# Performance work log

Hardware: AMD Instinct MI355X
Metric: run time of the kernel (lower is better)

## Reference

```python
import jax, jax.numpy as jnp
import numpy as np
from jax import lax

N_CLASS = 20
N_BOX = 2
GRID = 56          # n_cell_hw derived from input width: 56*56*(2*5+20) = 94080
BATCH = 256
SCORE_THRESH = 0.1 # hard-coded in _preds_filte
IOU_THRESH = 0.4   # hard-coded in _preds_filte
MAX_OUT = 30       # max_output_size
NMS_CAND = 256     # pre-select top candidates per image before O(K^2) NMS


def setup_inputs() -> dict:
    key = jax.random.key(0)
    D = GRID * GRID * (N_BOX * 5 + N_CLASS)
    net_outs = jax.random.uniform(key, (BATCH, D), dtype=jnp.float32)
    return {"net_outs": net_outs}


def _decode(net_outs):
    # Faithful port of _net_outs_parse (wh_sqrt=True)
    B = net_outs.shape[0]
    S, nb, C = GRID, N_BOX, N_CLASS
    bd1 = C * S * S
    bd2 = bd1 + nb * S * S
    cell_c = net_outs[:, :bd1].reshape(B, S, S, C)
    conf = net_outs[:, bd1:bd2].reshape(B, S, S, nb)
    coord = net_outs[:, bd2:].reshape(B, S, S, nb, 4)
    t_xy, t_wh = coord[..., :2], coord[..., 2:]
    # mesh_grid: w_index varies along axis 1, h_index along axis 0, stacked as (w, h)
    X, Y = jnp.meshgrid(jnp.arange(S, dtype=net_outs.dtype),
                        jnp.arange(S, dtype=net_outs.dtype), indexing='xy')
    grid = jnp.stack([X, Y], axis=-1)[:, :, None, :]  # [S,S,1,2]
    xy = (t_xy + grid) / S
    wh = jnp.square(t_wh)  # wh_sqrt=True
    mn = xy - wh * 0.5
    mx = xy + wh * 0.5
    # boxes_corner = [ymin, xmin, ymax, xmax]
    corners = jnp.concatenate([mn[..., 1:2], mn[..., 0:1], mx[..., 1:2], mx[..., 0:1]], axis=-1)
    c_probs = jnp.broadcast_to(cell_c[:, :, :, None, :], (B, S, S, nb, C))
    return jnp.concatenate([corners, conf[..., None], c_probs], axis=-1)  # [B,S,S,nb,5+C]


def _pairwise_iou(b):
    ymin, xmin, ymax, xmax = b[:, 0], b[:, 1], b[:, 2], b[:, 3]
    area = jnp.maximum(ymax - ymin, 0.0) * jnp.maximum(xmax - xmin, 0.0)
    iy = jnp.maximum(0.0, jnp.minimum(ymax[:, None], ymax[None, :]) - jnp.maximum(ymin[:, None], ymin[None, :]))
    ix = jnp.maximum(0.0, jnp.minimum(xmax[:, None], xmax[None, :]) - jnp.maximum(xmin[:, None], xmin[None, :]))
    inter = iy * ix
    union = area[:, None] + area[None, :] - inter
    return jnp.where(union > 0.0, inter / union, 0.0)


def _nms_image(item):
    # item: [N, 6] = (ymin, xmin, ymax, xmax, score, class)
    scores = item[:, 4]
    _, top_i = lax.top_k(scores, NMS_CAND)   # candidate pre-selection (greedy NMS only ever picks highest scores)
    cand = item[top_i]                       # [K, 6]
    iou = _pairwise_iou(cand[:, :4])         # [K, K]
    neg = jnp.finfo(item.dtype).min

    def step(valid, _):
        m = jnp.where(valid, cand[:, 4], neg)
        idx = jnp.argmax(m)
        ok = valid[idx]
        valid = valid & (iou[idx] <= IOU_THRESH)
        valid = valid.at[idx].set(False)
        return valid, (idx, ok)

    _, (idxs, ok) = lax.scan(step, jnp.ones(NMS_CAND, dtype=bool), None, length=MAX_OUT)
    rows = cand[idxs] * ok[:, None].astype(item.dtype)  # invalid slots -> zero rows (== pad with 0)
    _, oi = lax.top_k(rows[:, 4], MAX_OUT)               # sort by score desc, like tf.nn.top_k on padded preds
    return rows[oi]


def reference(net_outs):
    preds = _decode(net_outs)                    # [B,S,S,nb,25]
    B = preds.shape[0]
    cls_score = preds[..., 4:5] * preds[..., 5:]  # conf * class probs  [B,S,S,nb,C]
    cls = jnp.argmax(cls_score, axis=-1).astype(preds.dtype)
    s = jnp.max(cls_score, axis=-1)
    s = jnp.where(s >= SCORE_THRESH, s, 0.0)
    items = jnp.concatenate([preds[..., :4], s[..., None], cls[..., None]], axis=-1)
    items = items.reshape(B, -1, 6)              # [B, S*S*nb, 6]
    return jax.vmap(_nms_image)(items)           # [B, MAX_OUT, 6]
```

## Files before the change

kernel.cpp:

```cpp
#include <hip/hip_runtime.h>
#include <stdint.h>

#define S      56
#define NC     20
#define NCELL  (S*S)
#define NBOXES (NCELL*2)
#define DIM    94080
#define BD1    62720
#define BD2    68992
#define CAND   256
#define MAXOUT 30
#define NTHR   1024
#define NWAVE  16
#define NBIN   8192
#define CAP    512

__global__ __launch_bounds__(NTHR) void det_kernel(const float* __restrict__ in,
                                                   float* __restrict__ out) {
#pragma clang fp contract(off)
    const int b    = blockIdx.x;
    const int tid  = threadIdx.x;
    const int lane = tid & 63;
    const int wv   = tid >> 6;
    const float* img = in + (size_t)b * DIM;

    __shared__ uint32_t hist[NBIN];
    __shared__ uint32_t wsum[NWAVE];
    __shared__ int      bstar_s;
    __shared__ int      nsel;
    __shared__ uint64_t skey[CAP];
    __shared__ uint64_t ssort[CAND];
    __shared__ float cymin[CAND], cxmin[CAND], cymax[CAND], cxmax[CAND];
    __shared__ float carea[CAND], cscore[CAND], ccls[CAND];
    __shared__ int   klist[MAXOUT];
    __shared__ float rowbuf[MAXOUT * 6];

    ((uint4*)hist)[tid]        = uint4{0,0,0,0};
    ((uint4*)hist)[tid + NTHR] = uint4{0,0,0,0};
    if (tid == 0) nsel = 0;
    if (tid < MAXOUT) klist[tid] = -1;

    uint64_t key[4][2];
    bool     vld[4];
    #pragma unroll
    for (int i = 0; i < 4; i++) {
        int cell = tid + NTHR * i;
        vld[i] = (cell < NCELL);
        key[i][0] = key[i][1] = 0;
        if (vld[i]) {
            const float4* pv = (const float4*)(img + cell * NC);
            float p[NC];
            #pragma unroll
            for (int q = 0; q < 5; q++) {
                float4 v = pv[q];
                p[4*q+0] = v.x; p[4*q+1] = v.y; p[4*q+2] = v.z; p[4*q+3] = v.w;
            }
            float2 cf = *(const float2*)(img + BD1 + cell * 2);
            #pragma unroll
            for (int bb = 0; bb < 2; bb++) {
                float conf = bb ? cf.y : cf.x;
                float best = conf * p[0];
                int   cls  = 0;
                #pragma unroll
                for (int c = 1; c < NC; c++) {
                    float v = conf * p[c];
                    if (v > best) { best = v; cls = c; }
                }
                uint32_t sb = (best >= 0.1f) ? __float_as_uint(best) : 0u;
                int idx = cell * 2 + bb;
                key[i][bb] = ((uint64_t)sb << 18) | ((uint64_t)(8191 - idx) << 5)
                           | (uint64_t)cls;
            }
        }
    }
    __syncthreads();

    #pragma unroll
    for (int i = 0; i < 4; i++) {
        #pragma unroll
        for (int bb = 0; bb < 2; bb++) {
            uint32_t sb = (uint32_t)(key[i][bb] >> 18);
            if (vld[i] && sb != 0u) atomicAdd(&hist[sb >> 17], 1u);
            unsigned long long zm = __ballot(vld[i] && sb == 0u);
            if (lane == 0 && zm) atomicAdd(&hist[0], (uint32_t)__popcll(zm));
        }
    }
    __syncthreads();

    uint4 h0 = ((const uint4*)hist)[2*tid];
    uint4 h1 = ((const uint4*)hist)[2*tid+1];
    uint32_t hsum = h0.x+h0.y+h0.z+h0.w + h1.x+h1.y+h1.z+h1.w;
    uint32_t v = hsum;
    #pragma unroll
    for (int off = 1; off < 64; off <<= 1) {
        uint32_t u = __shfl_down(v, off);
        if (lane + off < 64) v += u;
    }
    if (lane == 0) wsum[wv] = v;
    __syncthreads();
    uint32_t add = 0;
    for (int w = wv + 1; w < NWAVE; w++) add += wsum[w];
    uint32_t Sm    = v + add;
    uint32_t above = Sm - hsum;
    if (above < CAND && CAND <= Sm) {
        uint32_t hh[8] = {h1.w, h1.z, h1.y, h1.x, h0.w, h0.z, h0.y, h0.x};
        uint32_t g = above;
        int bsel = 8 * tid;
        #pragma unroll
        for (int j = 0; j < 8; j++) {
            if (g + hh[j] >= CAND) { bsel = 8 * tid + (7 - j); break; }
            g += hh[j];
        }
        bstar_s = bsel;
    }
    __syncthreads();
    const uint32_t bstar = (uint32_t)bstar_s;

    #pragma unroll
    for (int i = 0; i < 4; i++) {
        #pragma unroll
        for (int bb = 0; bb < 2; bb++) {
            bool pred = vld[i] && ((uint32_t)(key[i][bb] >> 35) >= bstar);
            unsigned long long mask = __ballot(pred);
            if (mask) {
                int leader = __ffsll(mask) - 1;
                int base = 0;
                if (lane == leader) base = atomicAdd(&nsel, (int)__popcll(mask));
                base = __shfl(base, leader);
                if (pred) {
                    int pos = base + (int)__popcll(mask & ((1ull << lane) - 1ull));
                    if (pos < CAP) skey[pos] = key[i][bb];
                }
            }
        }
    }
    __syncthreads();

    const int M = (nsel < CAP) ? nsel : CAP;
    if (tid < M) {
        uint64_t my = skey[tid];
        int r = 0;
        #pragma unroll 4
        for (int j = 0; j < M; j++) r += (skey[j] > my);
        if (r < CAND) ssort[r] = my;
    }
    __syncthreads();

    if (tid < CAND) {
        uint64_t k = ssort[tid];
        int idx      = 8191 - (int)((k >> 5) & 0x1FFF);
        int cls      = (int)(k & 31u);
        uint32_t sb  = (uint32_t)(k >> 18);
        int cell = idx >> 1, bb = idx & 1;
        int i = cell / S, j = cell - i * S;
        float4 co = *(const float4*)(img + BD2 + cell * 8 + bb * 4);
        float x  = (co.x + (float)j) / 56.0f;
        float y  = (co.y + (float)i) / 56.0f;
        float wx = co.z * co.z;
        float wy = co.w * co.w;
        float hx = wx * 0.5f, hy = wy * 0.5f;
        float xmin = x - hx, ymin = y - hy, xmax = x + hx, ymax = y + hy;
        cymin[tid] = ymin; cxmin[tid] = xmin; cymax[tid] = ymax; cxmax[tid] = xmax;
        carea[tid] = fmaxf(ymax - ymin, 0.0f) * fmaxf(xmax - xmin, 0.0f);
        cscore[tid] = __uint_as_float(sb);
        ccls[tid]   = (float)cls;
    }
    __syncthreads();

    if (wv == 0) {
        float bym[4], bxm[4], byM[4], bxM[4], bar[4];
        #pragma unroll
        for (int s = 0; s < 4; s++) {
            int c = 4 * lane + s;
            bym[s] = cymin[c]; bxm[s] = cxmin[c];
            byM[s] = cymax[c]; bxM[s] = cxmax[c]; bar[s] = carea[c];
        }
        unsigned vmask = 0xFu;
        for (int it = 0; it < MAXOUT; it++) {
            unsigned long long mk = __ballot(vmask != 0u);
            if (!mk) break;
            int l0 = __ffsll(mk) - 1;
            int vb = __shfl((int)vmask, l0);
            int p  = 4 * l0 + (__ffs(vb) - 1);
            if (lane == 0) klist[it] = p;
            float pym = cymin[p], pxm = cxmin[p];
            float pyM = cymax[p], pxM = cxmax[p], par = carea[p];
            #pragma unroll
            for (int s = 0; s < 4; s++) {
                int c = 4 * lane + s;
                float iy = fmaxf(0.0f, fminf(pyM, byM[s]) - fmaxf(pym, bym[s]));
                float ix = fmaxf(0.0f, fminf(pxM, bxM[s]) - fmaxf(pxm, bxm[s]));
                float inter = iy * ix;
                float uni   = par + bar[s] - inter;
                float iou   = (uni > 0.0f) ? (inter / uni) : 0.0f;
                if (c == p || !(iou <= 0.4f)) vmask &= ~(1u << s);
            }
        }
    }
    __syncthreads();

    if (tid < MAXOUT) {
        int p = klist[tid];
        float* r = &rowbuf[tid * 6];
        if (p >= 0) {
            r[0] = cymin[p]; r[1] = cxmin[p]; r[2] = cymax[p];
            r[3] = cxmax[p]; r[4] = cscore[p]; r[5] = ccls[p];
        } else {
            r[0] = r[1] = r[2] = r[3] = r[4] = r[5] = 0.0f;
        }
    }
    __syncthreads();
    float* ob = out + (size_t)b * (MAXOUT * 6);
    if (tid < MAXOUT * 6) ob[tid] = rowbuf[tid];
}

extern "C" void kernel_launch(void* const* d_in, const int* in_sizes, int n_in,
                              void* d_out, int out_size, void* d_ws, size_t ws_size,
                              hipStream_t stream) {
    const float* in  = (const float*)d_in[0];
    float*       out = (float*)d_out;
    const int B = in_sizes[0] / DIM;
    det_kernel<<<dim3(B), dim3(NTHR), 0, stream>>>(in, out);
}
```

Measured before the change: 160.1 us.

## Split per-cell decode into a separate wide-grid kernel writing keys to workspace

Moves the per-cell class-score decode and key packing into its own kernel, launched over many small blocks per image. The keys are written to workspace, and the NMS kernel reads them back instead of decoding from the raw input. This targets the limited parallelism of one 1024-thread block per image during the bandwidth-heavy decode phase. In exchange it adds a second launch and an extra global write and read of the packed keys, and it falls back to the old path when the workspace is too small.

```diff
diff --git a/kernel.cpp b/kernel.cpp
--- a/kernel.cpp
+++ b/kernel.cpp
@@ -14,8 +14,53 @@
 #define NWAVE  16
 #define NBIN   8192
 #define CAP    512
-
+#define K1THR  256
+
+__device__ __forceinline__ void decode_cell(const float* __restrict__ img, int cell,
+                                            uint64_t& k0, uint64_t& k1) {
+#pragma clang fp contract(off)
+    const float4* pv = (const float4*)(img + cell * NC);
+    float p[NC];
+    #pragma unroll
+    for (int q = 0; q < 5; q++) {
+        float4 v = pv[q];
+        p[4*q+0] = v.x; p[4*q+1] = v.y; p[4*q+2] = v.z; p[4*q+3] = v.w;
+    }
+    float2 cf = *(const float2*)(img + BD1 + cell * 2);
+    uint64_t kk[2];
+    #pragma unroll
+    for (int bb = 0; bb < 2; bb++) {
+        float conf = bb ? cf.y : cf.x;
+        float best = conf * p[0];
+        int   cls  = 0;
+        #pragma unroll
+        for (int c = 1; c < NC; c++) {
+            float v = conf * p[c];
+            if (v > best) { best = v; cls = c; }
+        }
+        uint32_t sb = (best >= 0.1f) ? __float_as_uint(best) : 0u;
+        int idx = cell * 2 + bb;
+        kk[bb] = ((uint64_t)sb << 18) | ((uint64_t)(8191 - idx) << 5) | (uint64_t)cls;
+    }
+    k0 = kk[0]; k1 = kk[1];
+}
+
+__global__ __launch_bounds__(K1THR) void decode_kernel(const float* __restrict__ in,
+                                                       uint64_t* __restrict__ keys) {
+#pragma clang fp contract(off)
+    const int cell = blockIdx.x * K1THR + threadIdx.x;
+    const int b    = blockIdx.y;
+    if (cell >= NCELL) return;
+    const float* img = in + (size_t)b * DIM;
+    uint64_t k0, k1;
+    decode_cell(img, cell, k0, k1);
+    ulonglong2 st; st.x = k0; st.y = k1;
+    *(ulonglong2*)(keys + (size_t)b * NBOXES + (size_t)cell * 2) = st;
+}
+
+template<bool FROMKEYS>
 __global__ __launch_bounds__(NTHR) void det_kernel(const float* __restrict__ in,
+                                                   const uint64_t* __restrict__ keys,
                                                    float* __restrict__ out) {
 #pragma clang fp contract(off)
     const int b    = blockIdx.x;
@@ -42,34 +87,18 @@
 
     uint64_t key[4][2];
     bool     vld[4];
+    const uint64_t* kb = FROMKEYS ? (keys + (size_t)b * NBOXES) : nullptr;
     #pragma unroll
     for (int i = 0; i < 4; i++) {
         int cell = tid + NTHR * i;
         vld[i] = (cell < NCELL);
         key[i][0] = key[i][1] = 0;
         if (vld[i]) {
-            const float4* pv = (const float4*)(img + cell * NC);
-            float p[NC];
-            #pragma unroll
-            for (int q = 0; q < 5; q++) {
-                float4 v = pv[q];
-                p[4*q+0] = v.x; p[4*q+1] = v.y; p[4*q+2] = v.z; p[4*q+3] = v.w;
-            }
-            float2 cf = *(const float2*)(img + BD1 + cell * 2);
-            #pragma unroll
-            for (int bb = 0; bb < 2; bb++) {
-                float conf = bb ? cf.y : cf.x;
-                float best = conf * p[0];
-                int   cls  = 0;
-                #pragma unroll
-                for (int c = 1; c < NC; c++) {
-                    float v = conf * p[c];
-                    if (v > best) { best = v; cls = c; }
-                }
-                uint32_t sb = (best >= 0.1f) ? __float_as_uint(best) : 0u;
-                int idx = cell * 2 + bb;
-                key[i][bb] = ((uint64_t)sb << 18) | ((uint64_t)(8191 - idx) << 5)
-                           | (uint64_t)cls;
+            if (FROMKEYS) {
+                ulonglong2 v = *(const ulonglong2*)(kb + (size_t)cell * 2);
+                key[i][0] = v.x; key[i][1] = v.y;
+            } else {
+                decode_cell(img, cell, key[i][0], key[i][1]);
             }
         }
     }
@@ -220,5 +249,13 @@
     const float* in  = (const float*)d_in[0];
     float*       out = (float*)d_out;
     const int B = in_sizes[0] / DIM;
-    det_kernel<<<dim3(B), dim3(NTHR), 0, stream>>>(in, out);
-}
+    const size_t keys_bytes = (size_t)B * NBOXES * sizeof(uint64_t);
+
+    if (d_ws != nullptr && ws_size >= keys_bytes) {
+        uint64_t* keys = (uint64_t*)d_ws;
+        decode_kernel<<<dim3((NCELL + K1THR - 1) / K1THR, B), dim3(K1THR), 0, stream>>>(in, keys);
+        det_kernel<true><<<dim3(B), dim3(NTHR), 0, stream>>>(in, keys, out);
+    } else {
+        det_kernel<false><<<dim3(B), dim3(NTHR), 0, stream>>>(in, nullptr, out);
+    }
+}
```

Measured after the change: 162.4 us. No clear change (+1.4%).
